# Optimization experiments

Measured on AMD Instinct MI355X. Metric: run time of the kernel, lower is better.

## Reference

```python
import jax, jax.numpy as jnp
import numpy as np

N_EXPERTS = 16
TOP_K = int(N_EXPERTS * 0.2)  # = 3, matches int(self.n_experts * self.fraction_experts)
EPS = 1e-12  # F.normalize default eps


def setup_inputs() -> dict:
    key = jax.random.key(0)
    ks = jax.random.split(key, 6)
    B, T, D, H, E = 4, 1024, 1024, 2048, N_EXPERTS
    x = jax.random.normal(ks[0], (B, T, D), dtype=jnp.float32)
    gate = jax.random.normal(ks[1], (D, E), dtype=jnp.float32)
    # Experts: per-expert 2-layer MLP (Linear -> ReLU -> Linear), scaled init
    W1 = jax.random.normal(ks[2], (E, D, H), dtype=jnp.float32) * (1.0 / np.sqrt(D))
    b1 = jax.random.normal(ks[3], (E, H), dtype=jnp.float32) * 0.02
    W2 = jax.random.normal(ks[4], (E, H, D), dtype=jnp.float32) * (1.0 / np.sqrt(H))
    b2 = jax.random.normal(ks[5], (E, D), dtype=jnp.float32) * 0.02
    return {"x": x, "gate": gate, "W1": W1, "b1": b1, "W2": W2, "b2": b2}


def reference(x, gate, W1, b1, W2, b2):
    # Gating: softmax over experts
    raw_gate = jax.nn.softmax(jnp.einsum('btd,de->bte', x, gate), axis=-1)  # [B,T,E]
    # Top-k mask (value-based; sorted flag irrelevant for the mask)
    _, topk_idx = jax.lax.top_k(raw_gate, TOP_K)                  # [B,T,k]
    mask = jax.nn.one_hot(topk_idx, raw_gate.shape[-1],
                          dtype=raw_gate.dtype).sum(axis=2)      # [B,T,E]
    gate_topk = mask * raw_gate
    # L1 normalize over expert dim (F.normalize, p=1)
    gate_topk = gate_topk / jnp.maximum(
        jnp.sum(jnp.abs(gate_topk), axis=-1, keepdims=True), EPS)
    # Dense all-experts compute: expert_e(x) = relu(x@W1_e + b1_e)@W2_e + b2_e
    hidden = jax.nn.relu(jnp.einsum('btd,edh->bteh', x, W1) + b1)         # [B,T,E,H]
    expert_out = jnp.einsum('bteh,ehd->bted', hidden, W2) + b2            # [B,T,E,D]
    # Weighted combine
    return jnp.einsum('bte,bted->btd', gate_topk, expert_out)             # [B,T,D]
```

## Files before the change

kernel.cpp:

```cpp
#include <hip/hip_runtime.h>
#include <hip/hip_bf16.h>
#include <cstdio>

#define NTOK 4096
#define DDIM 1024
#define HDIM 2048
#define NEXP 16
#define NPAIR (NTOK * 3)
#define BM 128
#define MAXT1 112
#define MAXT2 112

typedef __bf16 bf16x8 __attribute__((ext_vector_type(8)));
typedef float f32x4 __attribute__((ext_vector_type(4)));
typedef unsigned short ushort8v __attribute__((ext_vector_type(8)));

#define OFF_TOPKE 4096
#define OFF_TOPKW 53248
#define OFF_PERM 102400
#define OFF_PW 151552
#define OFF_XB 262144
#define OFF_HID_F 8650752
#define OFF_W1T 58982400
#define OFF_W2T 126091264
#define NEED_FAST 193200128ull
#define OFF_HID_S 262144
#define NEED_SLOW 50593792ull

__device__ __forceinline__ unsigned short f2bf(float f) {
    __bf16 h = (__bf16)f;
    return __builtin_bit_cast(unsigned short, h);
}

typedef const __attribute__((address_space(1))) unsigned int* as1_u32p;
typedef __attribute__((address_space(3))) unsigned int* as3_u32p;
__device__ __forceinline__ void gload16(const void* g, void* l) {
    __builtin_amdgcn_global_load_lds((as1_u32p)g, (as3_u32p)l, 16, 0, 0);
}

__global__ void k_gating(const float* __restrict__ x, const float* __restrict__ gate,
                         int* __restrict__ topk_e, float* __restrict__ topk_w,
                         int* __restrict__ counts, unsigned short* __restrict__ xb) {
    const int t = blockIdx.x;
    const int l = threadIdx.x;
    const int e = l & 15, grp = l >> 4;
    const float* xr = x + (size_t)t * DDIM;
    double s = 0.0;
    const int d0 = grp * 256;
    for (int d = d0; d < d0 + 256; d += 4) {
        float4 xv = *(const float4*)(xr + d);
        if (xb && e == 0) {
            ushort4 pk;
            pk.x = f2bf(xv.x); pk.y = f2bf(xv.y); pk.z = f2bf(xv.z); pk.w = f2bf(xv.w);
            *(ushort4*)&xb[(size_t)t * DDIM + d] = pk;
        }
        s += (double)xv.x * (double)gate[(d + 0) * NEXP + e];
        s += (double)xv.y * (double)gate[(d + 1) * NEXP + e];
        s += (double)xv.z * (double)gate[(d + 2) * NEXP + e];
        s += (double)xv.w * (double)gate[(d + 3) * NEXP + e];
    }
    s += __shfl_xor(s, 16);
    s += __shfl_xor(s, 32);
    double cur = s;
    double lsel[3];
    int esel[3];
#pragma unroll
    for (int j = 0; j < 3; ++j) {
        double mx = cur;
#pragma unroll
        for (int off = 8; off >= 1; off >>= 1) {
            double o = __shfl_xor(mx, off);
            mx = (o > mx) ? o : mx;
        }
        unsigned long long b = __ballot(cur == mx);
        int sel = (__ffsll(b) - 1) & 15;
        esel[j] = sel;
        lsel[j] = mx;
        if (e == sel) cur = -1.0e300;
    }
    float w0 = 1.0f;
    float w1 = expf((float)(lsel[1] - lsel[0]));
    float w2 = expf((float)(lsel[2] - lsel[0]));
    float inv = 1.0f / (w0 + w1 + w2);
    if (l < 3) {
        float wv = (l == 0) ? w0 : (l == 1) ? w1 : w2;
        topk_e[t * 3 + l] = esel[l];
        topk_w[t * 3 + l] = wv * inv;
        atomicAdd(&counts[esel[l]], 1);
    }
}

__global__ void k_scan(int* __restrict__ meta) {
    if (threadIdx.x != 0) return;
    int* counts = meta;
    int* offs = meta + 16;
    int* cursor = meta + 48;
    int acc = 0;
    for (int e = 0; e < NEXP; ++e) {
        offs[e] = acc;
        cursor[e] = acc;
        acc += counts[e];
    }
    offs[NEXP] = acc;
    int nt = 0;
    for (int e = 0; e < NEXP; ++e)
        for (int r = offs[e]; r < offs[e + 1]; r += BM) {
            meta[128 + nt] = e;
            meta[256 + nt] = r;
            ++nt;
        }
    meta[64] = nt;
}

__global__ void k_scatter(const int* __restrict__ topk_e, const float* __restrict__ topk_w,
                          int* __restrict__ cursor, int* __restrict__ perm,
                          float* __restrict__ pw) {
    int t = blockIdx.x * blockDim.x + threadIdx.x;
    if (t >= NTOK) return;
#pragma unroll
    for (int j = 0; j < 3; ++j) {
        int e = topk_e[t * 3 + j];
        int pos = atomicAdd(&cursor[e], 1);
        perm[pos] = t;
        pw[pos] = topk_w[t * 3 + j];
    }
}

template <int K, int N, int NTILES, int KTILES>
__global__ __launch_bounds__(256) void k_convW(const float* __restrict__ W,
                                               unsigned short* __restrict__ Wt) {
    __shared__ unsigned short Ls[32 * 132];
    const int b = blockIdx.x;
    const int kt = b % KTILES;
    const int nt = (b / KTILES) % NTILES;
    const int e = b / (KTILES * NTILES);
    const int tid = threadIdx.x;
#pragma unroll
    for (int q = 0; q < 4; ++q) {
        int idx = q * 256 + tid;
        int k = idx >> 5, hg = idx & 31;
        const float* src = W + ((size_t)e * K + kt * 32 + k) * N + nt * 128 + hg * 4;
        float4 v = *(const float4*)src;
        ushort4 pk;
        pk.x = f2bf(v.x); pk.y = f2bf(v.y); pk.z = f2bf(v.z); pk.w = f2bf(v.w);
        *(ushort4*)&Ls[k * 132 + hg * 4] = pk;
    }
    __syncthreads();
    unsigned short* outb = Wt + (size_t)b * 4096;
#pragma unroll
    for (int q = 0; q < 2; ++q) {
        int cidx = q * 256 + tid;
        int r = cidx >> 2, c = cidx & 3;
        int cs = c ^ ((r >> 1) & 3);
        ushort8v v;
#pragma unroll
        for (int i = 0; i < 8; ++i) v[i] = Ls[(8 * cs + i) * 132 + r];
        *(ushort8v*)&outb[cidx * 8] = v;
    }
}

__global__ __launch_bounds__(256) void k_gemm1_f(const unsigned short* __restrict__ xb,
                                                 const unsigned short* __restrict__ W1t,
                                                 const float* __restrict__ b1,
                                                 const int* __restrict__ meta,
                                                 const int* __restrict__ perm,
                                                 unsigned short* __restrict__ hidden) {
    const int b = blockIdx.x;
    const int wg = (b & 7) * 224 + (b >> 3);
    const int mt = wg % MAXT1;
    const int y = wg / MAXT1;
    if (mt >= meta[64]) return;
    const int e = meta[128 + mt];
    const int r0 = meta[256 + mt];
    const int limit = meta[16 + e + 1] - r0;

    __shared__ unsigned short As_l[4096];
    __shared__ unsigned short Bs_l[4096];

    const int tid = threadIdx.x;
    const int lane = tid & 63, wave = tid >> 6;
    const int wr = wave >> 1, wc = wave & 1;

    size_t abase[2];
    size_t bbase[2];
#pragma unroll
    for (int q = 0; q < 2; ++q) {
        int cidx = q * 256 + tid;
        int r = cidx >> 2, c = cidx & 3;
        int cs = c ^ ((r >> 1) & 3);
        int rr = r0 + r; if (rr > NPAIR - 1) rr = NPAIR - 1;
        abase[q] = (size_t)perm[rr] * (DDIM * 2) + (size_t)cs * 16;
        bbase[q] = ((size_t)((e * 16 + y) * 32)) * 8192 + (size_t)cidx * 16;
    }
    const char* xb_b = (const char*)xb;
    const char* w_b = (const char*)W1t;

    f32x4 acc[4][4];
#pragma unroll
    for (int i = 0; i < 4; ++i)
#pragma unroll
        for (int j = 0; j < 4; ++j) acc[i][j] = (f32x4){0.f, 0.f, 0.f, 0.f};

    for (int kt = 0; kt < DDIM / 32; ++kt) {
        __syncthreads();
#pragma unroll
        for (int q = 0; q < 2; ++q) {
            gload16(xb_b + abase[q] + (size_t)kt * 64, &As_l[(q * 256 + wave * 64) * 8]);
            gload16(w_b + bbase[q] + (size_t)kt * 8192, &Bs_l[(q * 256 + wave * 64) * 8]);
        }
        __syncthreads();
        bf16x8 af[4], bfr[4];
#pragma unroll
        for (int m = 0; m < 4; ++m) {
            int r = wr * 64 + m * 16 + (lane & 15);
            int cc = ((lane >> 4) ^ ((r >> 1) & 3)) * 8;
            af[m] = *(const bf16x8*)&As_l[r * 32 + cc];
        }
#pragma unroll
        for (int n = 0; n < 4; ++n) {
            int r = wc * 64 + n * 16 + (lane & 15);
            int cc = ((lane >> 4) ^ ((r >> 1) & 3)) * 8;
            bfr[n] = *(const bf16x8*)&Bs_l[r * 32 + cc];
        }
#pragma unroll
        for (int m = 0; m < 4; ++m)
#pragma unroll
            for (int n = 0; n < 4; ++n)
                acc[m][n] = __builtin_amdgcn_mfma_f32_16x16x32_bf16(af[m], bfr[n], acc[m][n], 0, 0, 0);
    }

    const int h0 = y * 128;
    float bias[4];
#pragma unroll
    for (int n = 0; n < 4; ++n)
        bias[n] = b1[(size_t)e * HDIM + h0 + wc * 64 + n * 16 + (lane & 15)];
#pragma unroll
    for (int m = 0; m < 4; ++m)
#pragma unroll
        for (int j = 0; j < 4; ++j) {
            int row = wr * 64 + m * 16 + (lane >> 4) * 4 + j;
            if (row < limit) {
                size_t base = (size_t)(r0 + row) * HDIM + h0;
#pragma unroll
                for (int n = 0; n < 4; ++n) {
                    int col = wc * 64 + n * 16 + (lane & 15);
                    float v = acc[m][n][j] + bias[n];
                    hidden[base + col] = f2bf(fmaxf(v, 0.f));
                }
            }
        }
}

__global__ __launch_bounds__(256) void k_gemm2_f(const unsigned short* __restrict__ hidden,
                                                 const unsigned short* __restrict__ W2t,
                                                 const float* __restrict__ b2,
                                                 const int* __restrict__ meta,
                                                 const int* __restrict__ perm,
                                                 const float* __restrict__ pw,
                                                 float* __restrict__ out) {
    const int b = blockIdx.x;
    const int wg = (b & 7) * 112 + (b >> 3);
    const int mt = wg % MAXT2;
    const int y = wg / MAXT2;
    if (mt >= meta[64]) return;
    const int e = meta[128 + mt];
    const int r0 = meta[256 + mt];
    const int limit = meta[16 + e + 1] - r0;

    __shared__ unsigned short As_l[4096];
    __shared__ unsigned short Bs_l[4096];

    const int tid = threadIdx.x;
    const int lane = tid & 63, wave = tid >> 6;
    const int wr = wave >> 1, wc = wave & 1;

    size_t abase[2];
    size_t bbase[2];
#pragma unroll
    for (int q = 0; q < 2; ++q) {
        int cidx = q * 256 + tid;
        int r = cidx >> 2, c = cidx & 3;
        int cs = c ^ ((r >> 1) & 3);
        int rr = r0 + r; if (rr > NPAIR - 1) rr = NPAIR - 1;
        abase[q] = (size_t)rr * (HDIM * 2) + (size_t)cs * 16;
        bbase[q] = ((size_t)((e * 8 + y) * 64)) * 8192 + (size_t)cidx * 16;
    }
    const char* h_b = (const char*)hidden;
    const char* w_b = (const char*)W2t;

    f32x4 acc[4][4];
#pragma unroll
    for (int i = 0; i < 4; ++i)
#pragma unroll
        for (int j = 0; j < 4; ++j) acc[i][j] = (f32x4){0.f, 0.f, 0.f, 0.f};

    for (int kt = 0; kt < HDIM / 32; ++kt) {
        __syncthreads();
#pragma unroll
        for (int q = 0; q < 2; ++q) {
            gload16(h_b + abase[q] + (size_t)kt * 64, &As_l[(q * 256 + wave * 64) * 8]);
            gload16(w_b + bbase[q] + (size_t)kt * 8192, &Bs_l[(q * 256 + wave * 64) * 8]);
        }
        __syncthreads();
        bf16x8 af[4], bfr[4];
#pragma unroll
        for (int m = 0; m < 4; ++m) {
            int r = wr * 64 + m * 16 + (lane & 15);
            int cc = ((lane >> 4) ^ ((r >> 1) & 3)) * 8;
            af[m] = *(const bf16x8*)&As_l[r * 32 + cc];
        }
#pragma unroll
        for (int n = 0; n < 4; ++n) {
            int r = wc * 64 + n * 16 + (lane & 15);
            int cc = ((lane >> 4) ^ ((r >> 1) & 3)) * 8;
            bfr[n] = *(const bf16x8*)&Bs_l[r * 32 + cc];
        }
#pragma unroll
        for (int m = 0; m < 4; ++m)
#pragma unroll
            for (int n = 0; n < 4; ++n)
                acc[m][n] = __builtin_amdgcn_mfma_f32_16x16x32_bf16(af[m], bfr[n], acc[m][n], 0, 0, 0);
    }

    const int n0 = y * 128;
    float bias[4];
#pragma unroll
    for (int n = 0; n < 4; ++n)
        bias[n] = b2[(size_t)e * DDIM + n0 + wc * 64 + n * 16 + (lane & 15)];
#pragma unroll
    for (int m = 0; m < 4; ++m)
#pragma unroll
        for (int j = 0; j < 4; ++j) {
            int row = wr * 64 + m * 16 + (lane >> 4) * 4 + j;
            if (row < limit) {
                int tok = perm[r0 + row];
                float w = pw[r0 + row];
#pragma unroll
                for (int n = 0; n < 4; ++n) {
                    int col = wc * 64 + n * 16 + (lane & 15);
                    float v = (acc[m][n][j] + bias[n]) * w;
                    atomicAdd(&out[(size_t)tok * DDIM + n0 + col], v);
                }
            }
        }
}

__global__ __launch_bounds__(256) void k_gemm1_s(const float* __restrict__ x,
                                                 const float* __restrict__ W1,
                                                 const float* __restrict__ b1,
                                                 const int* __restrict__ meta,
                                                 const int* __restrict__ perm,
                                                 unsigned short* __restrict__ hidden) {
    const int mt = blockIdx.x;
    if (mt >= meta[64]) return;
    const int e = meta[128 + mt];
    const int r0 = meta[256 + mt];
    const int limit = meta[16 + e + 1] - r0;
    const int h0 = blockIdx.y * 128;

    __shared__ unsigned short As[128][40];
    __shared__ unsigned short Bs[128][40];

    const int tid = threadIdx.x;
    const int lane = tid & 63, wave = tid >> 6;
    const int wr = wave >> 1, wc = wave & 1;
    const int arow = tid >> 1, ahalf = tid & 1;
    const float* aptr = nullptr;
    if (arow < limit) aptr = x + (size_t)perm[r0 + arow] * DDIM + ahalf * 16;

    f32x4 acc[4][4];
#pragma unroll
    for (int i = 0; i < 4; ++i)
#pragma unroll
        for (int j = 0; j < 4; ++j) acc[i][j] = (f32x4){0.f, 0.f, 0.f, 0.f};

    for (int k0 = 0; k0 < DDIM; k0 += 32) {
        __syncthreads();
#pragma unroll
        for (int i = 0; i < 4; ++i) {
            float4 v = make_float4(0.f, 0.f, 0.f, 0.f);
            if (aptr) v = *(const float4*)(aptr + k0 + i * 4);
            ushort4 pk;
            pk.x = f2bf(v.x); pk.y = f2bf(v.y); pk.z = f2bf(v.z); pk.w = f2bf(v.w);
            *(ushort4*)&As[arow][ahalf * 16 + i * 4] = pk;
        }
#pragma unroll
        for (int it = 0; it < 2; ++it) {
            int s = tid + it * 256;
            int kp = s >> 5, cg = s & 31;
            const float* bp = W1 + ((size_t)e * DDIM + k0 + 2 * kp) * HDIM + h0 + cg * 4;
            float4 v0 = *(const float4*)bp;
            float4 v1 = *(const float4*)(bp + HDIM);
#pragma unroll
            for (int c = 0; c < 4; ++c) {
                unsigned int u = ((unsigned)f2bf(((const float*)&v1)[c]) << 16) |
                                 f2bf(((const float*)&v0)[c]);
                *(unsigned int*)&Bs[cg * 4 + c][2 * kp] = u;
            }
        }
        __syncthreads();
        bf16x8 af[4], bfr[4];
#pragma unroll
        for (int m = 0; m < 4; ++m)
            af[m] = *(const bf16x8*)&As[wr * 64 + m * 16 + (lane & 15)][(lane >> 4) * 8];
#pragma unroll
        for (int n = 0; n < 4; ++n)
            bfr[n] = *(const bf16x8*)&Bs[wc * 64 + n * 16 + (lane & 15)][(lane >> 4) * 8];
#pragma unroll
        for (int m = 0; m < 4; ++m)
#pragma unroll
            for (int n = 0; n < 4; ++n)
                acc[m][n] = __builtin_amdgcn_mfma_f32_16x16x32_bf16(af[m], bfr[n], acc[m][n], 0, 0, 0);
    }

    float bias[4];
#pragma unroll
    for (int n = 0; n < 4; ++n)
        bias[n] = b1[(size_t)e * HDIM + h0 + wc * 64 + n * 16 + (lane & 15)];
#pragma unroll
    for (int m = 0; m < 4; ++m)
#pragma unroll
        for (int j = 0; j < 4; ++j) {
            int row = wr * 64 + m * 16 + (lane >> 4) * 4 + j;
            if (row < limit) {
                size_t base = (size_t)(r0 + row) * HDIM + h0;
#pragma unroll
                for (int n = 0; n < 4; ++n) {
                    int col = wc * 64 + n * 16 + (lane & 15);
                    float v = acc[m][n][j] + bias[n];
                    hidden[base + col] = f2bf(fmaxf(v, 0.f));
                }
            }
        }
}

__global__ __launch_bounds__(256) void k_gemm2_s(const unsigned short* __restrict__ hidden,
                                                 const float* __restrict__ W2,
                                                 const float* __restrict__ b2,
                                                 const int* __restrict__ meta,
                                                 const int* __restrict__ perm,
                                                 const float* __restrict__ pw,
                                                 float* __restrict__ out) {
    const int mt = blockIdx.x;
    if (mt >= meta[64]) return;
    const int e = meta[128 + mt];
    const int r0 = meta[256 + mt];
    const int limit = meta[16 + e + 1] - r0;
    const int n0 = blockIdx.y * 128;

    __shared__ unsigned short As[128][40];
    __shared__ unsigned short Bs[128][40];

    const int tid = threadIdx.x;
    const int lane = tid & 63, wave = tid >> 6;
    const int wr = wave >> 1, wc = wave & 1;
    const int arow = tid >> 1, ahalf = tid & 1;
    const unsigned short* aptr = nullptr;
    if (arow < limit) aptr = hidden + (size_t)(r0 + arow) * HDIM + ahalf * 16;

    f32x4 acc[4][4];
#pragma unroll
    for (int i = 0; i < 4; ++i)
#pragma unroll
        for (int j = 0; j < 4; ++j) acc[i][j] = (f32x4){0.f, 0.f, 0.f, 0.f};

    for (int k0 = 0; k0 < HDIM; k0 += 32) {
        __syncthreads();
#pragma unroll
        for (int i = 0; i < 2; ++i) {
            uint4 v = make_uint4(0u, 0u, 0u, 0u);
            if (aptr) v = *(const uint4*)(aptr + k0 + i * 8);
            *(uint4*)&As[arow][ahalf * 16 + i * 8] = v;
        }
#pragma unroll
        for (int it = 0; it < 2; ++it) {
            int s = tid + it * 256;
            int kp = s >> 5, cg = s & 31;
            const float* bp = W2 + ((size_t)e * HDIM + k0 + 2 * kp) * DDIM + n0 + cg * 4;
            float4 v0 = *(const float4*)bp;
            float4 v1 = *(const float4*)(bp + DDIM);
#pragma unroll
            for (int c = 0; c < 4; ++c) {
                unsigned int u = ((unsigned)f2bf(((const float*)&v1)[c]) << 16) |
                                 f2bf(((const float*)&v0)[c]);
                *(unsigned int*)&Bs[cg * 4 + c][2 * kp] = u;
            }
        }
        __syncthreads();
        bf16x8 af[4], bfr[4];
#pragma unroll
        for (int m = 0; m < 4; ++m)
            af[m] = *(const bf16x8*)&As[wr * 64 + m * 16 + (lane & 15)][(lane >> 4) * 8];
#pragma unroll
        for (int n = 0; n < 4; ++n)
            bfr[n] = *(const bf16x8*)&Bs[wc * 64 + n * 16 + (lane & 15)][(lane >> 4) * 8];
#pragma unroll
        for (int m = 0; m < 4; ++m)
#pragma unroll
            for (int n = 0; n < 4; ++n)
                acc[m][n] = __builtin_amdgcn_mfma_f32_16x16x32_bf16(af[m], bfr[n], acc[m][n], 0, 0, 0);
    }

    float bias[4];
#pragma unroll
    for (int n = 0; n < 4; ++n)
        bias[n] = b2[(size_t)e * DDIM + n0 + wc * 64 + n * 16 + (lane & 15)];
#pragma unroll
    for (int m = 0; m < 4; ++m)
#pragma unroll
        for (int j = 0; j < 4; ++j) {
            int row = wr * 64 + m * 16 + (lane >> 4) * 4 + j;
            if (row < limit) {
                int tok = perm[r0 + row];
                float w = pw[r0 + row];
#pragma unroll
                for (int n = 0; n < 4; ++n) {
                    int col = wc * 64 + n * 16 + (lane & 15);
                    float v = (acc[m][n][j] + bias[n]) * w;
                    atomicAdd(&out[(size_t)tok * DDIM + n0 + col], v);
                }
            }
        }
}

extern "C" void kernel_launch(void* const* d_in, const int* in_sizes, int n_in,
                              void* d_out, int out_size, void* d_ws, size_t ws_size,
                              hipStream_t stream) {
    const float* x = (const float*)d_in[0];
    const float* gate = (const float*)d_in[1];
    const float* W1 = (const float*)d_in[2];
    const float* b1 = (const float*)d_in[3];
    const float* W2 = (const float*)d_in[4];
    const float* b2 = (const float*)d_in[5];
    float* out = (float*)d_out;

    const bool fast = ws_size >= NEED_FAST;
    if (!fast && ws_size < NEED_SLOW) {
        fprintf(stderr, "SparseKMoE: ws_size %zu too small\n", ws_size);
        return;
    }
    char* ws = (char*)d_ws;
    int* meta = (int*)ws;
    int* topk_e = (int*)(ws + OFF_TOPKE);
    float* topk_w = (float*)(ws + OFF_TOPKW);
    int* perm = (int*)(ws + OFF_PERM);
    float* pw = (float*)(ws + OFF_PW);
    unsigned short* xb = (unsigned short*)(ws + OFF_XB);
    unsigned short* hidden = (unsigned short*)(ws + (fast ? OFF_HID_F : OFF_HID_S));
    unsigned short* W1t = (unsigned short*)(ws + OFF_W1T);
    unsigned short* W2t = (unsigned short*)(ws + OFF_W2T);

    hipMemsetAsync(meta, 0, 4096, stream);
    hipMemsetAsync(d_out, 0, (size_t)NTOK * DDIM * sizeof(float), stream);

    k_gating<<<NTOK, 64, 0, stream>>>(x, gate, topk_e, topk_w, meta, fast ? xb : nullptr);
    k_scan<<<1, 64, 0, stream>>>(meta);
    k_scatter<<<16, 256, 0, stream>>>(topk_e, topk_w, meta + 48, perm, pw);

    if (fast) {
        k_convW<DDIM, HDIM, 16, 32><<<NEXP * 16 * 32, 256, 0, stream>>>(W1, W1t);
        k_convW<HDIM, DDIM, 8, 64><<<NEXP * 8 * 64, 256, 0, stream>>>(W2, W2t);
        k_gemm1_f<<<MAXT1 * 16, 256, 0, stream>>>(xb, W1t, b1, meta, perm, hidden);
        k_gemm2_f<<<MAXT2 * 8, 256, 0, stream>>>(hidden, W2t, b2, meta, perm, pw, out);
    } else {
        dim3 g1(MAXT1, HDIM / 128);
        k_gemm1_s<<<g1, 256, 0, stream>>>(x, W1, b1, meta, perm, hidden);
        dim3 g2(MAXT2, DDIM / 128);
        k_gemm2_s<<<g2, 256, 0, stream>>>(hidden, W2, b2, meta, perm, pw, out);
    }
}
```

Measured before the change: 676.3 us.

## Double-buffer LDS tiles in both expert GEMM kernels to overlap loads with MFMA

Both grouped GEMM kernels now keep two LDS buffers for A and B tiles. The loads for the next k-tile are issued before the MFMAs on the current tile, and each iteration ends with one barrier instead of two. The aim is to hide global-to-LDS latency behind compute and halve the barrier count. LDS use doubles to 32KB per block, which may reduce occupancy. Correctness depends on gload16 being an asynchronous direct-to-LDS load that the barrier's waitcnt covers.

```diff
diff --git a/kernel.cpp b/kernel.cpp
--- a/kernel.cpp
+++ b/kernel.cpp
@@ -174,8 +174,8 @@
     const int r0 = meta[256 + mt];
     const int limit = meta[16 + e + 1] - r0;
 
-    __shared__ unsigned short As_l[4096];
-    __shared__ unsigned short Bs_l[4096];
+    __shared__ unsigned short As_l[2][4096];
+    __shared__ unsigned short Bs_l[2][4096];
 
     const int tid = threadIdx.x;
     const int lane = tid & 63, wave = tid >> 6;
@@ -201,32 +201,44 @@
 #pragma unroll
         for (int j = 0; j < 4; ++j) acc[i][j] = (f32x4){0.f, 0.f, 0.f, 0.f};
 
-    for (int kt = 0; kt < DDIM / 32; ++kt) {
-        __syncthreads();
-#pragma unroll
-        for (int q = 0; q < 2; ++q) {
-            gload16(xb_b + abase[q] + (size_t)kt * 64, &As_l[(q * 256 + wave * 64) * 8]);
-            gload16(w_b + bbase[q] + (size_t)kt * 8192, &Bs_l[(q * 256 + wave * 64) * 8]);
-        }
-        __syncthreads();
+    const int NKT = DDIM / 32;
+#pragma unroll
+    for (int q = 0; q < 2; ++q) {
+        gload16(xb_b + abase[q], &As_l[0][(q * 256 + wave * 64) * 8]);
+        gload16(w_b + bbase[q], &Bs_l[0][(q * 256 + wave * 64) * 8]);
+    }
+    __syncthreads();
+
+    for (int kt = 0; kt < NKT; ++kt) {
+        const int cur = kt & 1;
+        if (kt + 1 < NKT) {
+#pragma unroll
+            for (int q = 0; q < 2; ++q) {
+                gload16(xb_b + abase[q] + (size_t)(kt + 1) * 64,
+                        &As_l[cur ^ 1][(q * 256 + wave * 64) * 8]);
+                gload16(w_b + bbase[q] + (size_t)(kt + 1) * 8192,
+                        &Bs_l[cur ^ 1][(q * 256 + wave * 64) * 8]);
+            }
+        }
         bf16x8 af[4], bfr[4];
 #pragma unroll
         for (int m = 0; m < 4; ++m) {
             int r = wr * 64 + m * 16 + (lane & 15);
             int cc = ((lane >> 4) ^ ((r >> 1) & 3)) * 8;
-            af[m] = *(const bf16x8*)&As_l[r * 32 + cc];
+            af[m] = *(const bf16x8*)&As_l[cur][r * 32 + cc];
         }
 #pragma unroll
         for (int n = 0; n < 4; ++n) {
             int r = wc * 64 + n * 16 + (lane & 15);
             int cc = ((lane >> 4) ^ ((r >> 1) & 3)) * 8;
-            bfr[n] = *(const bf16x8*)&Bs_l[r * 32 + cc];
+            bfr[n] = *(const bf16x8*)&Bs_l[cur][r * 32 + cc];
         }
 #pragma unroll
         for (int m = 0; m < 4; ++m)
 #pragma unroll
             for (int n = 0; n < 4; ++n)
                 acc[m][n] = __builtin_amdgcn_mfma_f32_16x16x32_bf16(af[m], bfr[n], acc[m][n], 0, 0, 0);
+        __syncthreads();
     }
 
     const int h0 = y * 128;
@@ -267,8 +279,8 @@
     const int r0 = meta[256 + mt];
     const int limit = meta[16 + e + 1] - r0;
 
-    __shared__ unsigned short As_l[4096];
-    __shared__ unsigned short Bs_l[4096];
+    __shared__ unsigned short As_l[2][4096];
+    __shared__ unsigned short Bs_l[2][4096];
 
     const int tid = threadIdx.x;
     const int lane = tid & 63, wave = tid >> 6;
@@ -294,32 +306,44 @@
 #pragma unroll
         for (int j = 0; j < 4; ++j) acc[i][j] = (f32x4){0.f, 0.f, 0.f, 0.f};
 
-    for (int kt = 0; kt < HDIM / 32; ++kt) {
-        __syncthreads();
-#pragma unroll
-        for (int q = 0; q < 2; ++q) {
-            gload16(h_b + abase[q] + (size_t)kt * 64, &As_l[(q * 256 + wave * 64) * 8]);
-            gload16(w_b + bbase[q] + (size_t)kt * 8192, &Bs_l[(q * 256 + wave * 64) * 8]);
-        }
-        __syncthreads();
+    const int NKT = HDIM / 32;
+#pragma unroll
+    for (int q = 0; q < 2; ++q) {
+        gload16(h_b + abase[q], &As_l[0][(q * 256 + wave * 64) * 8]);
+        gload16(w_b + bbase[q], &Bs_l[0][(q * 256 + wave * 64) * 8]);
+    }
+    __syncthreads();
+
+    for (int kt = 0; kt < NKT; ++kt) {
+        const int cur = kt & 1;
+        if (kt + 1 < NKT) {
+#pragma unroll
+            for (int q = 0; q < 2; ++q) {
+                gload16(h_b + abase[q] + (size_t)(kt + 1) * 64,
+                        &As_l[cur ^ 1][(q * 256 + wave * 64) * 8]);
+                gload16(w_b + bbase[q] + (size_t)(kt + 1) * 8192,
+                        &Bs_l[cur ^ 1][(q * 256 + wave * 64) * 8]);
+            }
+        }
         bf16x8 af[4], bfr[4];
 #pragma unroll
         for (int m = 0; m < 4; ++m) {
             int r = wr * 64 + m * 16 + (lane & 15);
             int cc = ((lane >> 4) ^ ((r >> 1) & 3)) * 8;
-            af[m] = *(const bf16x8*)&As_l[r * 32 + cc];
+            af[m] = *(const bf16x8*)&As_l[cur][r * 32 + cc];
         }
 #pragma unroll
         for (int n = 0; n < 4; ++n) {
             int r = wc * 64 + n * 16 + (lane & 15);
             int cc = ((lane >> 4) ^ ((r >> 1) & 3)) * 8;
-            bfr[n] = *(const bf16x8*)&Bs_l[r * 32 + cc];
+            bfr[n] = *(const bf16x8*)&Bs_l[cur][r * 32 + cc];
         }
 #pragma unroll
         for (int m = 0; m < 4; ++m)
 #pragma unroll
             for (int n = 0; n < 4; ++n)
                 acc[m][n] = __builtin_amdgcn_mfma_f32_16x16x32_bf16(af[m], bfr[n], acc[m][n], 0, 0, 0);
+        __syncthreads();
     }
 
     const int n0 = y * 128;
```

After: 695.0 us. 2.8% more time.

## Double GEMM K-tile to 64 with wider swizzle, split-K gemm2, coalesce bf16 cast

Applied to the files above, without the earlier changes.

Both expert GEMMs now stage 64-wide K tiles (16 KB per operand in LDS) with an 8-way XOR swizzle, which halves the number of barrier-separated load/compute iterations. The weight conversion kernel is changed to emit the matching 64-row tile layout. gemm2 is split along K into two halves, doubling the grid; the extra atomics into the output apply the bias only in the first half. The x-to-bf16 cast in gating moves out of the single-lane-per-group path into a coalesced loop across all 64 lanes, at the cost of re-reading the row. Larger LDS tiles may reduce occupancy, and split-K doubles the atomic traffic to the output.

```diff
diff --git a/kernel.cpp b/kernel.cpp
--- a/kernel.cpp
+++ b/kernel.cpp
@@ -49,11 +49,6 @@
     const int d0 = grp * 256;
     for (int d = d0; d < d0 + 256; d += 4) {
         float4 xv = *(const float4*)(xr + d);
-        if (xb && e == 0) {
-            ushort4 pk;
-            pk.x = f2bf(xv.x); pk.y = f2bf(xv.y); pk.z = f2bf(xv.z); pk.w = f2bf(xv.w);
-            *(ushort4*)&xb[(size_t)t * DDIM + d] = pk;
-        }
         s += (double)xv.x * (double)gate[(d + 0) * NEXP + e];
         s += (double)xv.y * (double)gate[(d + 1) * NEXP + e];
         s += (double)xv.z * (double)gate[(d + 2) * NEXP + e];
@@ -61,6 +56,16 @@
     }
     s += __shfl_xor(s, 16);
     s += __shfl_xor(s, 32);
+    if (xb) {
+#pragma unroll
+        for (int i = 0; i < 4; ++i) {
+            int d = i * 256 + l * 4;
+            float4 v = *(const float4*)(xr + d);
+            ushort4 pk;
+            pk.x = f2bf(v.x); pk.y = f2bf(v.y); pk.z = f2bf(v.z); pk.w = f2bf(v.w);
+            *(ushort4*)&xb[(size_t)t * DDIM + d] = pk;
+        }
+    }
     double cur = s;
     double lsel[3];
     int esel[3];
@@ -129,29 +134,29 @@
 template <int K, int N, int NTILES, int KTILES>
 __global__ __launch_bounds__(256) void k_convW(const float* __restrict__ W,
                                                unsigned short* __restrict__ Wt) {
-    __shared__ unsigned short Ls[32 * 132];
+    __shared__ unsigned short Ls[64 * 132];
     const int b = blockIdx.x;
     const int kt = b % KTILES;
     const int nt = (b / KTILES) % NTILES;
     const int e = b / (KTILES * NTILES);
     const int tid = threadIdx.x;
 #pragma unroll
-    for (int q = 0; q < 4; ++q) {
+    for (int q = 0; q < 8; ++q) {
         int idx = q * 256 + tid;
         int k = idx >> 5, hg = idx & 31;
-        const float* src = W + ((size_t)e * K + kt * 32 + k) * N + nt * 128 + hg * 4;
+        const float* src = W + ((size_t)e * K + kt * 64 + k) * N + nt * 128 + hg * 4;
         float4 v = *(const float4*)src;
         ushort4 pk;
         pk.x = f2bf(v.x); pk.y = f2bf(v.y); pk.z = f2bf(v.z); pk.w = f2bf(v.w);
         *(ushort4*)&Ls[k * 132 + hg * 4] = pk;
     }
     __syncthreads();
-    unsigned short* outb = Wt + (size_t)b * 4096;
-#pragma unroll
-    for (int q = 0; q < 2; ++q) {
+    unsigned short* outb = Wt + (size_t)b * 8192;
+#pragma unroll
+    for (int q = 0; q < 4; ++q) {
         int cidx = q * 256 + tid;
-        int r = cidx >> 2, c = cidx & 3;
-        int cs = c ^ ((r >> 1) & 3);
+        int r = cidx >> 3, c = cidx & 7;
+        int cs = c ^ (r & 7);
         ushort8v v;
 #pragma unroll
         for (int i = 0; i < 8; ++i) v[i] = Ls[(8 * cs + i) * 132 + r];
@@ -174,23 +179,22 @@
     const int r0 = meta[256 + mt];
     const int limit = meta[16 + e + 1] - r0;
 
-    __shared__ unsigned short As_l[4096];
-    __shared__ unsigned short Bs_l[4096];
+    __shared__ unsigned short As_l[8192];
+    __shared__ unsigned short Bs_l[8192];
 
     const int tid = threadIdx.x;
     const int lane = tid & 63, wave = tid >> 6;
     const int wr = wave >> 1, wc = wave & 1;
 
-    size_t abase[2];
-    size_t bbase[2];
-#pragma unroll
-    for (int q = 0; q < 2; ++q) {
+    size_t abase[4], bbase[4];
+#pragma unroll
+    for (int q = 0; q < 4; ++q) {
         int cidx = q * 256 + tid;
-        int r = cidx >> 2, c = cidx & 3;
-        int cs = c ^ ((r >> 1) & 3);
+        int r = cidx >> 3, c = cidx & 7;
+        int cs = c ^ (r & 7);
         int rr = r0 + r; if (rr > NPAIR - 1) rr = NPAIR - 1;
         abase[q] = (size_t)perm[rr] * (DDIM * 2) + (size_t)cs * 16;
-        bbase[q] = ((size_t)((e * 16 + y) * 32)) * 8192 + (size_t)cidx * 16;
+        bbase[q] = (size_t)((e * 16 + y) * 16) * 16384 + (size_t)cidx * 16;
     }
     const char* xb_b = (const char*)xb;
     const char* w_b = (const char*)W1t;
@@ -201,32 +205,35 @@
 #pragma unroll
         for (int j = 0; j < 4; ++j) acc[i][j] = (f32x4){0.f, 0.f, 0.f, 0.f};
 
-    for (int kt = 0; kt < DDIM / 32; ++kt) {
-        __syncthreads();
-#pragma unroll
-        for (int q = 0; q < 2; ++q) {
-            gload16(xb_b + abase[q] + (size_t)kt * 64, &As_l[(q * 256 + wave * 64) * 8]);
-            gload16(w_b + bbase[q] + (size_t)kt * 8192, &Bs_l[(q * 256 + wave * 64) * 8]);
-        }
-        __syncthreads();
-        bf16x8 af[4], bfr[4];
-#pragma unroll
-        for (int m = 0; m < 4; ++m) {
-            int r = wr * 64 + m * 16 + (lane & 15);
-            int cc = ((lane >> 4) ^ ((r >> 1) & 3)) * 8;
-            af[m] = *(const bf16x8*)&As_l[r * 32 + cc];
-        }
-#pragma unroll
-        for (int n = 0; n < 4; ++n) {
-            int r = wc * 64 + n * 16 + (lane & 15);
-            int cc = ((lane >> 4) ^ ((r >> 1) & 3)) * 8;
-            bfr[n] = *(const bf16x8*)&Bs_l[r * 32 + cc];
-        }
-#pragma unroll
-        for (int m = 0; m < 4; ++m)
-#pragma unroll
-            for (int n = 0; n < 4; ++n)
-                acc[m][n] = __builtin_amdgcn_mfma_f32_16x16x32_bf16(af[m], bfr[n], acc[m][n], 0, 0, 0);
+    for (int kt = 0; kt < DDIM / 64; ++kt) {
+        __syncthreads();
+#pragma unroll
+        for (int q = 0; q < 4; ++q) {
+            gload16(xb_b + abase[q] + (size_t)kt * 128, &As_l[(q * 256 + wave * 64) * 8]);
+            gload16(w_b + bbase[q] + (size_t)kt * 16384, &Bs_l[(q * 256 + wave * 64) * 8]);
+        }
+        __syncthreads();
+#pragma unroll
+        for (int h = 0; h < 2; ++h) {
+            bf16x8 af[4], bfr[4];
+#pragma unroll
+            for (int m = 0; m < 4; ++m) {
+                int r = wr * 64 + m * 16 + (lane & 15);
+                int c = (h * 4 + (lane >> 4)) ^ (r & 7);
+                af[m] = *(const bf16x8*)&As_l[r * 64 + c * 8];
+            }
+#pragma unroll
+            for (int n = 0; n < 4; ++n) {
+                int r = wc * 64 + n * 16 + (lane & 15);
+                int c = (h * 4 + (lane >> 4)) ^ (r & 7);
+                bfr[n] = *(const bf16x8*)&Bs_l[r * 64 + c * 8];
+            }
+#pragma unroll
+            for (int m = 0; m < 4; ++m)
+#pragma unroll
+                for (int n = 0; n < 4; ++n)
+                    acc[m][n] = __builtin_amdgcn_mfma_f32_16x16x32_bf16(af[m], bfr[n], acc[m][n], 0, 0, 0);
+        }
     }
 
     const int h0 = y * 128;
@@ -259,31 +266,32 @@
                                                  const float* __restrict__ pw,
                                                  float* __restrict__ out) {
     const int b = blockIdx.x;
-    const int wg = (b & 7) * 112 + (b >> 3);
+    const int wg = (b & 7) * 224 + (b >> 3);
     const int mt = wg % MAXT2;
-    const int y = wg / MAXT2;
+    const int rest = wg / MAXT2;
+    const int y = rest & 7;
+    const int ks = rest >> 3;
     if (mt >= meta[64]) return;
     const int e = meta[128 + mt];
     const int r0 = meta[256 + mt];
     const int limit = meta[16 + e + 1] - r0;
 
-    __shared__ unsigned short As_l[4096];
-    __shared__ unsigned short Bs_l[4096];
+    __shared__ unsigned short As_l[8192];
+    __shared__ unsigned short Bs_l[8192];
 
     const int tid = threadIdx.x;
     const int lane = tid & 63, wave = tid >> 6;
     const int wr = wave >> 1, wc = wave & 1;
 
-    size_t abase[2];
-    size_t bbase[2];
-#pragma unroll
-    for (int q = 0; q < 2; ++q) {
+    size_t abase[4], bbase[4];
+#pragma unroll
+    for (int q = 0; q < 4; ++q) {
         int cidx = q * 256 + tid;
-        int r = cidx >> 2, c = cidx & 3;
-        int cs = c ^ ((r >> 1) & 3);
+        int r = cidx >> 3, c = cidx & 7;
+        int cs = c ^ (r & 7);
         int rr = r0 + r; if (rr > NPAIR - 1) rr = NPAIR - 1;
-        abase[q] = (size_t)rr * (HDIM * 2) + (size_t)cs * 16;
-        bbase[q] = ((size_t)((e * 8 + y) * 64)) * 8192 + (size_t)cidx * 16;
+        abase[q] = (size_t)rr * (HDIM * 2) + (size_t)ks * 2048 + (size_t)cs * 16;
+        bbase[q] = (size_t)((e * 8 + y) * 32 + ks * 16) * 16384 + (size_t)cidx * 16;
     }
     const char* h_b = (const char*)hidden;
     const char* w_b = (const char*)W2t;
@@ -294,32 +302,35 @@
 #pragma unroll
         for (int j = 0; j < 4; ++j) acc[i][j] = (f32x4){0.f, 0.f, 0.f, 0.f};
 
-    for (int kt = 0; kt < HDIM / 32; ++kt) {
-        __syncthreads();
-#pragma unroll
-        for (int q = 0; q < 2; ++q) {
-            gload16(h_b + abase[q] + (size_t)kt * 64, &As_l[(q * 256 + wave * 64) * 8]);
-            gload16(w_b + bbase[q] + (size_t)kt * 8192, &Bs_l[(q * 256 + wave * 64) * 8]);
-        }
-        __syncthreads();
-        bf16x8 af[4], bfr[4];
-#pragma unroll
-        for (int m = 0; m < 4; ++m) {
-            int r = wr * 64 + m * 16 + (lane & 15);
-            int cc = ((lane >> 4) ^ ((r >> 1) & 3)) * 8;
-            af[m] = *(const bf16x8*)&As_l[r * 32 + cc];
-        }
-#pragma unroll
-        for (int n = 0; n < 4; ++n) {
-            int r = wc * 64 + n * 16 + (lane & 15);
-            int cc = ((lane >> 4) ^ ((r >> 1) & 3)) * 8;
-            bfr[n] = *(const bf16x8*)&Bs_l[r * 32 + cc];
-        }
-#pragma unroll
-        for (int m = 0; m < 4; ++m)
-#pragma unroll
-            for (int n = 0; n < 4; ++n)
-                acc[m][n] = __builtin_amdgcn_mfma_f32_16x16x32_bf16(af[m], bfr[n], acc[m][n], 0, 0, 0);
+    for (int kt = 0; kt < 16; ++kt) {
+        __syncthreads();
+#pragma unroll
+        for (int q = 0; q < 4; ++q) {
+            gload16(h_b + abase[q] + (size_t)kt * 128, &As_l[(q * 256 + wave * 64) * 8]);
+            gload16(w_b + bbase[q] + (size_t)kt * 16384, &Bs_l[(q * 256 + wave * 64) * 8]);
+        }
+        __syncthreads();
+#pragma unroll
+        for (int h = 0; h < 2; ++h) {
+            bf16x8 af[4], bfr[4];
+#pragma unroll
+            for (int m = 0; m < 4; ++m) {
+                int r = wr * 64 + m * 16 + (lane & 15);
+                int c = (h * 4 + (lane >> 4)) ^ (r & 7);
+                af[m] = *(const bf16x8*)&As_l[r * 64 + c * 8];
+            }
+#pragma unroll
+            for (int n = 0; n < 4; ++n) {
+                int r = wc * 64 + n * 16 + (lane & 15);
+                int c = (h * 4 + (lane >> 4)) ^ (r & 7);
+                bfr[n] = *(const bf16x8*)&Bs_l[r * 64 + c * 8];
+            }
+#pragma unroll
+            for (int m = 0; m < 4; ++m)
+#pragma unroll
+                for (int n = 0; n < 4; ++n)
+                    acc[m][n] = __builtin_amdgcn_mfma_f32_16x16x32_bf16(af[m], bfr[n], acc[m][n], 0, 0, 0);
+        }
     }
 
     const int n0 = y * 128;
@@ -338,8 +349,8 @@
 #pragma unroll
                 for (int n = 0; n < 4; ++n) {
                     int col = wc * 64 + n * 16 + (lane & 15);
-                    float v = (acc[m][n][j] + bias[n]) * w;
-                    atomicAdd(&out[(size_t)tok * DDIM + n0 + col], v);
+                    float v = acc[m][n][j] + (ks == 0 ? bias[n] : 0.0f);
+                    atomicAdd(&out[(size_t)tok * DDIM + n0 + col], v * w);
                 }
             }
         }
@@ -558,10 +569,10 @@
     k_scatter<<<16, 256, 0, stream>>>(topk_e, topk_w, meta + 48, perm, pw);
 
     if (fast) {
-        k_convW<DDIM, HDIM, 16, 32><<<NEXP * 16 * 32, 256, 0, stream>>>(W1, W1t);
-        k_convW<HDIM, DDIM, 8, 64><<<NEXP * 8 * 64, 256, 0, stream>>>(W2, W2t);
+        k_convW<DDIM, HDIM, 16, 16><<<NEXP * 16 * 16, 256, 0, stream>>>(W1, W1t);
+        k_convW<HDIM, DDIM, 8, 32><<<NEXP * 8 * 32, 256, 0, stream>>>(W2, W2t);
         k_gemm1_f<<<MAXT1 * 16, 256, 0, stream>>>(xb, W1t, b1, meta, perm, hidden);
-        k_gemm2_f<<<MAXT2 * 8, 256, 0, stream>>>(hidden, W2t, b2, meta, perm, pw, out);
+        k_gemm2_f<<<MAXT2 * 16, 256, 0, stream>>>(hidden, W2t, b2, meta, perm, pw, out);
     } else {
         dim3 g1(MAXT1, HDIM / 128);
         k_gemm1_s<<<g1, 256, 0, stream>>>(x, W1, b1, meta, perm, hidden);
```

Result: faster. 651.8 us (-3.6%).
